# Kernel tuning notes

Hardware: AMD Instinct MI355X
Metric: run time of the kernel (lower is better)

## Reference

```python
import jax, jax.numpy as jnp
import numpy as np

N = 50000      # query points
M = 50000      # support points
KNN = 32       # neighbors per query
K = 15         # kernel points
C_IN = 64
C_OUT = 128
RADIUS = 2.5
KP_EXTENT = 1.2


def setup_inputs() -> dict:
    key = jax.random.key(0)
    ks = jax.random.split(key, 6)
    q_pts = jax.random.uniform(ks[0], (N, 3), dtype=jnp.float32)
    s_pts = jax.random.uniform(ks[1], (M, 3), dtype=jnp.float32)
    s_feats = jax.random.normal(ks[2], (M, C_IN), dtype=jnp.float32)
    # index M refers to the appended shadow point/feature row
    neigh_inds = jax.random.randint(ks[3], (N, KNN), 0, M + 1, dtype=jnp.int32)
    weights = jax.random.normal(ks[4], (K, C_IN, C_OUT), dtype=jnp.float32) * 0.05
    kernel_points = (jax.random.uniform(ks[5], (K, 3), dtype=jnp.float32) * 2.0 - 1.0) * RADIUS
    return {"q_pts": q_pts, "s_pts": s_pts, "s_feats": s_feats,
            "neigh_inds": neigh_inds, "weights": weights,
            "kernel_points": kernel_points}


def reference(q_pts, s_pts, s_feats, neigh_inds, weights, kernel_points):
    # append shadow point far away and zero shadow feature row
    s_pts_pad = jnp.concatenate([s_pts, jnp.full((1, 3), 1e6, s_pts.dtype)], axis=0)
    s_feats_pad = jnp.concatenate(
        [s_feats, jnp.zeros((1, s_feats.shape[1]), s_feats.dtype)], axis=0)

    neigh_pts = s_pts_pad[neigh_inds] - q_pts[:, None, :]       # (n, k, 3)
    neigh_feats = s_feats_pad[neigh_inds]                        # (n, k, c_in)

    diff = neigh_pts[:, :, None, :] - kernel_points[None, None]  # (n, k, K, 3)
    sq_dist = jnp.sum(diff * diff, axis=-1) + 1e-8               # (n, k, K)

    # linear kernel-point influence
    h = jnp.clip(1.0 - jnp.sqrt(sq_dist) / KP_EXTENT, 0.0)       # (n, k, K)

    # aggregate neighbor feats per kernel point, then apply per-kernel weights
    kernel_feats = jnp.einsum('nke,nkc->nec', h, neigh_feats)    # (n, K, c_in)
    q_feats = jnp.einsum('nec,eco->no', kernel_feats, weights)   # (n, c_out)

    # normalize by number of valid (non-shadow, sum>0) neighbors
    neighbor_num = jnp.sum(jnp.sum(neigh_feats, axis=-1) > 0, axis=-1)
    neighbor_num = jnp.maximum(neighbor_num, 1).astype(q_feats.dtype)[:, None]
    return q_feats / neighbor_num
```

## Files before the change

### kernel.cpp

```cpp
#include <hip/hip_runtime.h>


namespace {
constexpr int NQ   = 50000;
constexpr int MS   = 50000;
constexpr int KNN  = 32;
constexpr int KP   = 15;
constexpr int CIN  = 64;
constexpr int COUT = 128;
constexpr int QB   = 32;
constexpr int ROWS = KP * CIN;
constexpr int RND  = 3;
constexpr int RE   = 5;
constexpr int KBR  = (RE * CIN) / 32;
constexpr int KBT  = ROWS / 32;
constexpr int NT   = COUT / 16;
constexpr int ASTR = RE * CIN + 4;
constexpr float KP_EXT_INV = 1.0f / 1.2f;
constexpr size_t WS_HI   = 200704;
constexpr size_t WS_LO   = WS_HI + (size_t)ROWS * COUT * 2;
constexpr size_t WS_NEED = WS_LO + (size_t)ROWS * COUT * 2;
constexpr int OF_H   = 0;
constexpr int OF_DX  = 5280;
constexpr int OF_CPK = 6048;
constexpr int OF_KP  = 6304;
}

typedef __attribute__((ext_vector_type(8))) short short8;
typedef __attribute__((ext_vector_type(4))) float f32x4;
typedef __attribute__((ext_vector_type(4))) unsigned int u32x4;

__device__ __forceinline__ short f32_bf16(float x) {
    unsigned u = __builtin_bit_cast(unsigned, x);
    u = u + 0x7fffu + ((u >> 16) & 1u);
    return (short)(u >> 16);
}
__device__ __forceinline__ float bf16_f32(short h) {
    unsigned u = ((unsigned)(unsigned short)h) << 16;
    return __builtin_bit_cast(float, u);
}
__device__ __forceinline__ unsigned pack_hilo(float x) {
    unsigned xu = __builtin_bit_cast(unsigned, x);
    unsigned r  = xu + 0x7fffu + ((xu >> 16) & 1u);
    unsigned hi = r & 0xffff0000u;
    float lof = x - __builtin_bit_cast(float, hi);
    unsigned lu = __builtin_bit_cast(unsigned, lof);
    unsigned r2 = lu + 0x7fffu + ((lu >> 16) & 1u);
    return hi | (r2 >> 16);
}
__device__ __forceinline__ unsigned permb(unsigned a, unsigned b, unsigned sel) {
#if __has_builtin(__builtin_amdgcn_perm)
    return __builtin_amdgcn_perm(a, b, sel);
#else
    if (sel == 0x07060302u) return (a & 0xffff0000u) | (b >> 16);
    return (a << 16) | (b & 0xffffu);
#endif
}
__device__ __forceinline__ void unpack_a(uint4 a, uint4 b, short8& hi, short8& lo) {
    u32x4 h, l;
    h[0] = permb(a.y, a.x, 0x07060302u); l[0] = permb(a.y, a.x, 0x05040100u);
    h[1] = permb(a.w, a.z, 0x07060302u); l[1] = permb(a.w, a.z, 0x05040100u);
    h[2] = permb(b.y, b.x, 0x07060302u); l[2] = permb(b.y, b.x, 0x05040100u);
    h[3] = permb(b.w, b.z, 0x07060302u); l[3] = permb(b.w, b.z, 0x05040100u);
    hi = __builtin_bit_cast(short8, h);
    lo = __builtin_bit_cast(short8, l);
}

__global__ __launch_bounds__(256)
void prep_kernel(const float* __restrict__ s_feats, const float* __restrict__ W,
                 float* __restrict__ rs, short* __restrict__ whi, short* __restrict__ wlo)
{
    int b = blockIdx.x;
    if (b < 60) {
        int wv = threadIdx.x >> 6, lane = threadIdx.x & 63;
        int id = b * 4 + wv;
        int t = id / KBT, kb = id % KBT;
        short8 hi8, lo8;
        #pragma unroll
        for (int j = 0; j < 8; ++j) {
            int row = kb * 32 + ((lane >> 4) & 3) * 8 + j;
            int col = t * 16 + (lane & 15);
            float x = W[(size_t)row * COUT + col];
            short h = f32_bf16(x);
            hi8[j] = h;
            lo8[j] = f32_bf16(x - bf16_f32(h));
        }
        ((short8*)whi)[id * 64 + lane] = hi8;
        ((short8*)wlo)[id * 64 + lane] = lo8;
    } else {
        int tdx = (b - 60) * 256 + threadIdx.x;
        int row = tdx >> 3, l8 = tdx & 7;
        if (row < MS) {
            const float4* p = (const float4*)(s_feats + (size_t)row * CIN + l8 * 8);
            float4 a = p[0], c = p[1];
            float s = ((a.x + a.y) + (a.z + a.w)) + ((c.x + c.y) + (c.z + c.w));
            s += __shfl_xor(s, 1);
            s += __shfl_xor(s, 2);
            s += __shfl_xor(s, 4);
            if (l8 == 0) rs[row] = s;
        }
    }
}

__global__ __launch_bounds__(512, 4)
void kpconv_mfma(const float* __restrict__ q_pts,
                 const float* __restrict__ s_pts,
                 const float* __restrict__ s_feats,
                 const int*   __restrict__ neigh,
                 const float* __restrict__ kpts,
                 const float* __restrict__ rowsum,
                 const short* __restrict__ whi,
                 const short* __restrict__ wlo,
                 float*       __restrict__ out)
{
    __shared__ __align__(16) unsigned int smem[QB * ASTR];
    __shared__ float norm_s[QB];

    float* smf   = (float*)smem;
    const int tid  = threadIdx.x;
    const int lane = tid & 63;
    const int wv   = tid >> 6;
    const int blk  = blockIdx.x;
    const int k32  = lane & 31;
    const int half = lane >> 5;
    const int quad = lane >> 4;

    float* hbase = smf + OF_H + wv * 660;
    float* dx_b  = smf + OF_DX + wv * 96;
    int*   cpk   = (int*)(smf + OF_CPK) + wv * 32;
    float* kp_s  = smf + OF_KP;

    if (tid < KP * 3) kp_s[tid] = kpts[tid];
    if (lane < 20) hbase[640 + lane] = 0.0f;
    __syncthreads();

    float kfv[4][KP];

    #pragma unroll
    for (int j = 0; j < 4; ++j) {
        const int q  = wv * 4 + j;
        const int n  = blk * QB + q;
        const int nc = n < NQ ? n : NQ - 1;
        const float qx = q_pts[nc * 3 + 0];
        const float qy = q_pts[nc * 3 + 1];
        const float qz = q_pts[nc * 3 + 2];

        int idx = MS;
        bool flag = false;
        if (lane < KNN) {
            idx = neigh[nc * KNN + k32];
            bool valid = idx < MS;
            int  ic    = valid ? idx : MS - 1;
            float px = s_pts[ic * 3 + 0];
            float py = s_pts[ic * 3 + 1];
            float pz = s_pts[ic * 3 + 2];
            dx_b[k32 * 3 + 0] = valid ? px - qx : 1e6f;
            dx_b[k32 * 3 + 1] = valid ? py - qy : 1e6f;
            dx_b[k32 * 3 + 2] = valid ? pz - qz : 1e6f;
            flag = valid && (rowsum[ic] > 0.0f);
        }
        {
            unsigned long long b = __ballot(flag);
            int cnt = (int)__popcll(b);
            if (lane == 0) norm_s[q] = 1.0f / (float)(cnt > 1 ? cnt : 1);
        }
        __builtin_amdgcn_wave_barrier();

        const float dx = dx_b[k32 * 3 + 0];
        const float dy = dx_b[k32 * 3 + 1];
        const float dz = dx_b[k32 * 3 + 2];
        float om = 0.0f;
        #pragma unroll
        for (int p = 0; p < 8; ++p) {
            const int e = (p << 1) + half;
            if (e < KP) {
                float ax = dx - kp_s[e * 3 + 0];
                float ay = dy - kp_s[e * 3 + 1];
                float az = dz - kp_s[e * 3 + 2];
                float d2 = ax * ax + ay * ay + az * az + 1e-8f;
                float hh = 1.0f - sqrtf(d2) * KP_EXT_INV;
                hh = hh > 0.0f ? hh : 0.0f;
                hbase[k32 * 20 + e] = hh;
                om = fmaxf(om, hh);
            }
        }
        om = fmaxf(om, __shfl_xor(om, 32));
        unsigned int kmask = (unsigned int)__ballot(om > 0.0f);
        int nv = __popc(kmask);

        if (lane < KNN) {
            bool bit = (kmask >> k32) & 1u;
            int pos = bit ? __popc(kmask & ((1u << k32) - 1u))
                          : nv + __popc((~kmask) & ((1u << k32) - 1u));
            cpk[pos] = bit ? ((idx << 6) | k32) : 32;
        }
        __builtin_amdgcn_wave_barrier();

        #pragma unroll
        for (int e = 0; e < KP; ++e) kfv[j][e] = 0.0f;
        const int nvr = (nv + 3) & ~3;
        for (int base = 0; base < nvr; base += 4) {
            int pk[4];
            float nf[4];
            #pragma unroll
            for (int u = 0; u < 4; ++u) pk[u] = __builtin_amdgcn_readfirstlane(cpk[base + u]);
            #pragma unroll
            for (int u = 0; u < 4; ++u) nf[u] = s_feats[(size_t)(pk[u] >> 6) * CIN + lane];
            #pragma unroll
            for (int u = 0; u < 4; ++u) {
                const float4* hr = (const float4*)(hbase + (pk[u] & 63) * 20);
                float4 h0 = hr[0], h1 = hr[1], h2 = hr[2], h3 = hr[3];
                float f = nf[u];
                kfv[j][0]  += h0.x * f;  kfv[j][1]  += h0.y * f;
                kfv[j][2]  += h0.z * f;  kfv[j][3]  += h0.w * f;
                kfv[j][4]  += h1.x * f;  kfv[j][5]  += h1.y * f;
                kfv[j][6]  += h1.z * f;  kfv[j][7]  += h1.w * f;
                kfv[j][8]  += h2.x * f;  kfv[j][9]  += h2.y * f;
                kfv[j][10] += h2.z * f;  kfv[j][11] += h2.w * f;
                kfv[j][12] += h3.x * f;  kfv[j][13] += h3.y * f;
                kfv[j][14] += h3.z * f;
            }
        }
    }

    const short8* wh = (const short8*)whi;
    const short8* wl = (const short8*)wlo;
    f32x4 acc0 = {0.f, 0.f, 0.f, 0.f};
    f32x4 acc1 = {0.f, 0.f, 0.f, 0.f};
    const int qA = lane & 15;

    #pragma unroll
    for (int r = 0; r < RND; ++r) {
        __syncthreads();
        #pragma unroll
        for (int j = 0; j < 4; ++j) {
            const int q = wv * 4 + j;
            #pragma unroll
            for (int e5 = 0; e5 < RE; ++e5) {
                smem[q * ASTR + e5 * CIN + lane] = pack_hilo(kfv[j][r * RE + e5]);
            }
        }
        __syncthreads();

        #pragma unroll 2
        for (int kb = 0; kb < KBR; ++kb) {
            const uint4* a0p = (const uint4*)(smem + qA * ASTR + kb * 32 + quad * 8);
            uint4 a0 = a0p[0], a0b = a0p[1];
            const uint4* a1p = (const uint4*)(smem + (16 + qA) * ASTR + kb * 32 + quad * 8);
            uint4 a1 = a1p[0], a1b = a1p[1];
            short8 ah0, al0, ah1, al1;
            unpack_a(a0, a0b, ah0, al0);
            unpack_a(a1, a1b, ah1, al1);

            const int kbg = r * KBR + kb;
            short8 bh = wh[(wv * KBT + kbg) * 64 + lane];
            short8 bl = wl[(wv * KBT + kbg) * 64 + lane];

            acc0 = __builtin_amdgcn_mfma_f32_16x16x32_bf16(ah0, bh, acc0, 0, 0, 0);
            acc1 = __builtin_amdgcn_mfma_f32_16x16x32_bf16(ah1, bh, acc1, 0, 0, 0);
            acc0 = __builtin_amdgcn_mfma_f32_16x16x32_bf16(ah0, bl, acc0, 0, 0, 0);
            acc1 = __builtin_amdgcn_mfma_f32_16x16x32_bf16(ah1, bl, acc1, 0, 0, 0);
            acc0 = __builtin_amdgcn_mfma_f32_16x16x32_bf16(al0, bh, acc0, 0, 0, 0);
            acc1 = __builtin_amdgcn_mfma_f32_16x16x32_bf16(al1, bh, acc1, 0, 0, 0);
        }
    }

    const int oc = lane & 15;
    #pragma unroll
    for (int rr = 0; rr < 4; ++rr) {
        int qm0 = quad * 4 + rr;
        int qm1 = 16 + qm0;
        int n0 = blk * QB + qm0;
        int n1 = blk * QB + qm1;
        if (n0 < NQ) out[(size_t)n0 * COUT + wv * 16 + oc] = acc0[rr] * norm_s[qm0];
        if (n1 < NQ) out[(size_t)n1 * COUT + wv * 16 + oc] = acc1[rr] * norm_s[qm1];
    }
}

__global__ __launch_bounds__(256, 6)
void kpconv_fallback(const float* __restrict__ q_pts,
                     const float* __restrict__ s_pts,
                     const float* __restrict__ s_feats,
                     const int*   __restrict__ neigh,
                     const float* __restrict__ W,
                     const float* __restrict__ kpts,
                     float*       __restrict__ out)
{
    constexpr int QBF = 16, CHUNK_I = 320, NPAIR = 160;
    __shared__ __align__(16) float smem[NPAIR * 32];
    __shared__ float norm_s[QBF];
    float (*h_lds)[KNN][20] = (float (*)[KNN][20])smem;
    float (*dxyz)[KNN][3]   = (float (*)[KNN][3])(smem + 2560);
    int*   idxl             = (int*)(smem + 2944);
    float* kp_s             = smem + 3072;

    const int tid = threadIdx.x, lane = tid & 63, wv = tid >> 6, blk = blockIdx.x;
    const int k32 = lane & 31, half = lane >> 5;
    if (tid < KP * 3) kp_s[tid] = kpts[tid];
    __syncthreads();
    float kfv[4][KP];

    #pragma unroll
    for (int j = 0; j < 4; ++j) {
        const int q = wv * 4 + j, n = blk * QBF + q;
        const float qx = q_pts[n*3], qy = q_pts[n*3+1], qz = q_pts[n*3+2];
        if (lane < KNN) {
            int idx = neigh[n * KNN + k32];
            idxl[wv * KNN + k32] = idx;
            bool valid = idx < MS;
            int ic = valid ? idx : MS - 1;
            dxyz[wv][k32][0] = valid ? s_pts[ic*3]   - qx : 1e6f;
            dxyz[wv][k32][1] = valid ? s_pts[ic*3+1] - qy : 1e6f;
            dxyz[wv][k32][2] = valid ? s_pts[ic*3+2] - qz : 1e6f;
        }
        __builtin_amdgcn_wave_barrier();
        const float dx = dxyz[wv][k32][0], dy = dxyz[wv][k32][1], dz = dxyz[wv][k32][2];
        float om = 0.0f;
        #pragma unroll
        for (int p = 0; p < 8; ++p) {
            const int e = (p << 1) + half;
            if (e < KP) {
                float ax = dx - kp_s[e*3], ay = dy - kp_s[e*3+1], az = dz - kp_s[e*3+2];
                float hh = 1.0f - sqrtf(ax*ax + ay*ay + az*az + 1e-8f) * KP_EXT_INV;
                hh = hh > 0.0f ? hh : 0.0f;
                h_lds[wv][k32][e] = hh;
                om = fmaxf(om, hh);
            }
        }
        om = fmaxf(om, __shfl_xor(om, 32));
        unsigned int kmask = (unsigned int)__ballot(om > 0.0f);
        __builtin_amdgcn_wave_barrier();
        {
            int idx = idxl[wv * KNN + k32];
            bool valid = idx < MS;
            int ic = valid ? idx : MS - 1;
            const float4* rp = (const float4*)(s_feats + (size_t)ic * CIN + half * 32);
            float4 s4 = rp[0];
            #pragma unroll
            for (int t = 1; t < 8; ++t) { float4 a = rp[t]; s4.x+=a.x; s4.y+=a.y; s4.z+=a.z; s4.w+=a.w; }
            float s = (s4.x + s4.y) + (s4.z + s4.w);
            s += __shfl_xor(s, 32);
            unsigned long long b = __ballot(valid && (s > 0.0f));
            int cnt = (int)(__popcll(b) >> 1);
            if (lane == 0) norm_s[q] = 1.0f / (float)(cnt > 1 ? cnt : 1);
        }
        #pragma unroll
        for (int e = 0; e < KP; ++e) kfv[j][e] = 0.0f;
        unsigned int mk = kmask;
        while (mk) {
            int k = __builtin_ctz(mk); mk &= mk - 1;
            int idx2 = idxl[wv * KNN + k];
            int ic2 = idx2 < MS ? idx2 : MS - 1;
            float nf = s_feats[(size_t)ic2 * CIN + lane];
            const float4* hr = (const float4*)(&h_lds[wv][k][0]);
            float4 h0 = hr[0], h1 = hr[1], h2 = hr[2], h3 = hr[3];
            kfv[j][0]+=h0.x*nf; kfv[j][1]+=h0.y*nf; kfv[j][2]+=h0.z*nf; kfv[j][3]+=h0.w*nf;
            kfv[j][4]+=h1.x*nf; kfv[j][5]+=h1.y*nf; kfv[j][6]+=h1.z*nf; kfv[j][7]+=h1.w*nf;
            kfv[j][8]+=h2.x*nf; kfv[j][9]+=h2.y*nf; kfv[j][10]+=h2.z*nf; kfv[j][11]+=h2.w*nf;
            kfv[j][12]+=h3.x*nf; kfv[j][13]+=h3.y*nf; kfv[j][14]+=h3.z*nf;
        }
    }

    const int o4 = tid & 31, qi = tid >> 5, q0 = qi * 2, q1 = q0 + 1;
    float4 tot0 = make_float4(0,0,0,0), tot1 = make_float4(0,0,0,0);
    #pragma unroll
    for (int r = 0; r < 3; ++r) {
        __syncthreads();
        #pragma unroll
        for (int j = 0; j < 4; ++j) {
            const int q = wv * 4 + j;
            #pragma unroll
            for (int e5 = 0; e5 < 5; ++e5) {
                int i = e5 * CIN + lane, pr = i >> 1, m = pr & 14;
                smem[pr * 32 + ((q ^ m) << 1) + (i & 1)] = kfv[j][r * 5 + e5];
            }
        }
        __syncthreads();
        const float* wb = W + (size_t)(r * CHUNK_I) * COUT + (o4 << 2);
        float4 acc0 = make_float4(0,0,0,0), acc1 = make_float4(0,0,0,0);
        #pragma unroll 4
        for (int p = 0; p < NPAIR; ++p) {
            float4 kk = *(const float4*)(smem + p * 32 + ((q0 ^ (p & 14)) << 1));
            float4 w0 = *(const float4*)(wb + (size_t)(2*p) * COUT);
            float4 w1 = *(const float4*)(wb + (size_t)(2*p+1) * COUT);
            acc0.x+=w0.x*kk.x; acc0.y+=w0.y*kk.x; acc0.z+=w0.z*kk.x; acc0.w+=w0.w*kk.x;
            acc1.x+=w0.x*kk.z; acc1.y+=w0.y*kk.z; acc1.z+=w0.z*kk.z; acc1.w+=w0.w*kk.z;
            acc0.x+=w1.x*kk.y; acc0.y+=w1.y*kk.y; acc0.z+=w1.z*kk.y; acc0.w+=w1.w*kk.y;
            acc1.x+=w1.x*kk.w; acc1.y+=w1.y*kk.w; acc1.z+=w1.z*kk.w; acc1.w+=w1.w*kk.w;
        }
        tot0.x+=acc0.x; tot0.y+=acc0.y; tot0.z+=acc0.z; tot0.w+=acc0.w;
        tot1.x+=acc1.x; tot1.y+=acc1.y; tot1.z+=acc1.z; tot1.w+=acc1.w;
    }
    const float nm0 = norm_s[q0], nm1 = norm_s[q1];
    const size_t base = (size_t)(blk * QBF) * COUT + (o4 << 2);
    *(float4*)(out + base + (size_t)q0 * COUT) =
        make_float4(tot0.x*nm0, tot0.y*nm0, tot0.z*nm0, tot0.w*nm0);
    *(float4*)(out + base + (size_t)q1 * COUT) =
        make_float4(tot1.x*nm1, tot1.y*nm1, tot1.z*nm1, tot1.w*nm1);
}

extern "C" void kernel_launch(void* const* d_in, const int* in_sizes, int n_in,
                              void* d_out, int out_size, void* d_ws, size_t ws_size,
                              hipStream_t stream) {
    const float* q_pts   = (const float*)d_in[0];
    const float* s_pts   = (const float*)d_in[1];
    const float* s_feats = (const float*)d_in[2];
    const int*   neigh   = (const int*)d_in[3];
    const float* W       = (const float*)d_in[4];
    const float* kpts    = (const float*)d_in[5];
    float* outp = (float*)d_out;

    if (ws_size >= WS_NEED) {
        float* rs  = (float*)d_ws;
        short* whi = (short*)((char*)d_ws + WS_HI);
        short* wlo = (short*)((char*)d_ws + WS_LO);
        int rs_blocks = (MS * 8 + 255) / 256;
        hipLaunchKernelGGL(prep_kernel, dim3(60 + rs_blocks), dim3(256), 0, stream,
                           s_feats, W, rs, whi, wlo);
        hipLaunchKernelGGL(kpconv_mfma, dim3((NQ + QB - 1) / QB), dim3(512), 0, stream,
                           q_pts, s_pts, s_feats, neigh, kpts, rs, whi, wlo, outp);
    } else {
        hipLaunchKernelGGL(kpconv_fallback, dim3(NQ / 16), dim3(256), 0, stream,
                           q_pts, s_pts, s_feats, neigh, W, kpts, outp);
    }
}
```

Measured before the change: 163.8 us.

## Compute per-query kernel-point aggregation with bf16x3 MFMA instead of scalar FMAs

Replaces the scalar loop that accumulates influence times neighbor features with a 16x16x32 MFMA per query, using hi/lo bf16 splitting for near-fp32 accuracy. Influence weights are written transposed into shared memory, and neighbor feature rows are gathered per lane. A new prep kernel pre-packs all support features into hi/lo bf16 pairs in the workspace when it is large enough. This drops the neighbor-compaction skip of zero-influence neighbors and adds extra gather traffic and pack work in exchange for matrix-core throughput.

Result: slower. 207.5 us (+26.7%).

```diff
diff --git a/kernel.cpp b/kernel.cpp
--- a/kernel.cpp
+++ b/kernel.cpp
@@ -14,16 +14,19 @@
 constexpr int RE   = 5;
 constexpr int KBR  = (RE * CIN) / 32;
 constexpr int KBT  = ROWS / 32;
-constexpr int NT   = COUT / 16;
 constexpr int ASTR = RE * CIN + 4;
 constexpr float KP_EXT_INV = 1.0f / 1.2f;
-constexpr size_t WS_HI   = 200704;
-constexpr size_t WS_LO   = WS_HI + (size_t)ROWS * COUT * 2;
-constexpr size_t WS_NEED = WS_LO + (size_t)ROWS * COUT * 2;
-constexpr int OF_H   = 0;
-constexpr int OF_DX  = 5280;
-constexpr int OF_CPK = 6048;
-constexpr int OF_KP  = 6304;
+constexpr int OF_HT  = 0;
+constexpr int OF_DX  = 4608;
+constexpr int OF_IDX = 5376;
+constexpr int OF_KP  = 5632;
+constexpr size_t WSF_FPK = 200704;
+constexpr size_t WSF_HI  = WSF_FPK + (size_t)MS * CIN * 4;
+constexpr size_t WSF_LO  = WSF_HI + (size_t)ROWS * COUT * 2;
+constexpr size_t WSF_END = WSF_LO + (size_t)ROWS * COUT * 2;
+constexpr size_t WSB_HI  = 200704;
+constexpr size_t WSB_LO  = 446464;
+constexpr size_t WSB_END = 692224;
 }
 
 typedef __attribute__((ext_vector_type(8))) short short8;
@@ -56,7 +59,7 @@
     return (a << 16) | (b & 0xffffu);
 #endif
 }
-__device__ __forceinline__ void unpack_a(uint4 a, uint4 b, short8& hi, short8& lo) {
+__device__ __forceinline__ void unpack8(uint4 a, uint4 b, short8& hi, short8& lo) {
     u32x4 h, l;
     h[0] = permb(a.y, a.x, 0x07060302u); l[0] = permb(a.y, a.x, 0x05040100u);
     h[1] = permb(a.w, a.z, 0x07060302u); l[1] = permb(a.w, a.z, 0x05040100u);
@@ -67,8 +70,41 @@
 }
 
 __global__ __launch_bounds__(256)
-void prep_kernel(const float* __restrict__ s_feats, const float* __restrict__ W,
-                 float* __restrict__ rs, short* __restrict__ whi, short* __restrict__ wlo)
+void prep_full(const float* __restrict__ s_feats, const float* __restrict__ W,
+               float* __restrict__ rs, unsigned* __restrict__ fpk,
+               short* __restrict__ whi, short* __restrict__ wlo)
+{
+    int b = blockIdx.x;
+    if (b < 60) {
+        int wv = threadIdx.x >> 6, lane = threadIdx.x & 63;
+        int id = b * 4 + wv;
+        int t = id / KBT, kb = id % KBT;
+        short8 hi8, lo8;
+        #pragma unroll
+        for (int j = 0; j < 8; ++j) {
+            int row = kb * 32 + ((lane >> 4) & 3) * 8 + j;
+            int col = t * 16 + (lane & 15);
+            float x = W[(size_t)row * COUT + col];
+            short h = f32_bf16(x);
+            hi8[j] = h;
+            lo8[j] = f32_bf16(x - bf16_f32(h));
+        }
+        ((short8*)whi)[id * 64 + lane] = hi8;
+        ((short8*)wlo)[id * 64 + lane] = lo8;
+    } else {
+        int t = (b - 60) * 256 + threadIdx.x;
+        float x = s_feats[t];
+        fpk[t] = pack_hilo(x);
+        float s = x;
+        s += __shfl_xor(s, 1);  s += __shfl_xor(s, 2);  s += __shfl_xor(s, 4);
+        s += __shfl_xor(s, 8);  s += __shfl_xor(s, 16); s += __shfl_xor(s, 32);
+        if ((t & 63) == 0) rs[t >> 6] = s;
+    }
+}
+
+__global__ __launch_bounds__(256)
+void prep_basic(const float* __restrict__ s_feats, const float* __restrict__ W,
+                float* __restrict__ rs, short* __restrict__ whi, short* __restrict__ wlo)
 {
     int b = blockIdx.x;
     if (b < 60) {
@@ -102,6 +138,7 @@
     }
 }
 
+template<bool PREPACKED>
 __global__ __launch_bounds__(512, 4)
 void kpconv_mfma(const float* __restrict__ q_pts,
                  const float* __restrict__ s_pts,
@@ -109,6 +146,7 @@
                  const int*   __restrict__ neigh,
                  const float* __restrict__ kpts,
                  const float* __restrict__ rowsum,
+                 const unsigned* __restrict__ fpk,
                  const short* __restrict__ whi,
                  const short* __restrict__ wlo,
                  float*       __restrict__ out)
@@ -116,7 +154,7 @@
     __shared__ __align__(16) unsigned int smem[QB * ASTR];
     __shared__ float norm_s[QB];
 
-    float* smf   = (float*)smem;
+    float* smf = (float*)smem;
     const int tid  = threadIdx.x;
     const int lane = tid & 63;
     const int wv   = tid >> 6;
@@ -124,17 +162,17 @@
     const int k32  = lane & 31;
     const int half = lane >> 5;
     const int quad = lane >> 4;
-
-    float* hbase = smf + OF_H + wv * 660;
-    float* dx_b  = smf + OF_DX + wv * 96;
-    int*   cpk   = (int*)(smf + OF_CPK) + wv * 32;
-    float* kp_s  = smf + OF_KP;
+    const int c15  = lane & 15;
+
+    unsigned* hT  = smem + OF_HT + wv * 576;
+    float*    dxb = smf + OF_DX + wv * 96;
+    int*      idxl = (int*)(smf + OF_IDX) + wv * 32;
+    float*    kp_s = smf + OF_KP;
 
     if (tid < KP * 3) kp_s[tid] = kpts[tid];
-    if (lane < 20) hbase[640 + lane] = 0.0f;
     __syncthreads();
 
-    float kfv[4][KP];
+    unsigned pkf[4][4][4];
 
     #pragma unroll
     for (int j = 0; j < 4; ++j) {
@@ -145,18 +183,18 @@
         const float qy = q_pts[nc * 3 + 1];
         const float qz = q_pts[nc * 3 + 2];
 
-        int idx = MS;
         bool flag = false;
         if (lane < KNN) {
-            idx = neigh[nc * KNN + k32];
+            int idx = neigh[nc * KNN + k32];
             bool valid = idx < MS;
             int  ic    = valid ? idx : MS - 1;
+            idxl[k32] = ic;
             float px = s_pts[ic * 3 + 0];
             float py = s_pts[ic * 3 + 1];
             float pz = s_pts[ic * 3 + 2];
-            dx_b[k32 * 3 + 0] = valid ? px - qx : 1e6f;
-            dx_b[k32 * 3 + 1] = valid ? py - qy : 1e6f;
-            dx_b[k32 * 3 + 2] = valid ? pz - qz : 1e6f;
+            dxb[k32 * 3 + 0] = valid ? px - qx : 1e6f;
+            dxb[k32 * 3 + 1] = valid ? py - qy : 1e6f;
+            dxb[k32 * 3 + 2] = valid ? pz - qz : 1e6f;
             flag = valid && (rowsum[ic] > 0.0f);
         }
         {
@@ -166,10 +204,9 @@
         }
         __builtin_amdgcn_wave_barrier();
 
-        const float dx = dx_b[k32 * 3 + 0];
-        const float dy = dx_b[k32 * 3 + 1];
-        const float dz = dx_b[k32 * 3 + 2];
-        float om = 0.0f;
+        const float dx = dxb[k32 * 3 + 0];
+        const float dy = dxb[k32 * 3 + 1];
+        const float dz = dxb[k32 * 3 + 2];
         #pragma unroll
         for (int p = 0; p < 8; ++p) {
             const int e = (p << 1) + half;
@@ -180,46 +217,48 @@
                 float d2 = ax * ax + ay * ay + az * az + 1e-8f;
                 float hh = 1.0f - sqrtf(d2) * KP_EXT_INV;
                 hh = hh > 0.0f ? hh : 0.0f;
-                hbase[k32 * 20 + e] = hh;
-                om = fmaxf(om, hh);
+                hT[e * 36 + k32] = pack_hilo(hh);
             }
         }
-        om = fmaxf(om, __shfl_xor(om, 32));
-        unsigned int kmask = (unsigned int)__ballot(om > 0.0f);
-        int nv = __popc(kmask);
-
-        if (lane < KNN) {
-            bool bit = (kmask >> k32) & 1u;
-            int pos = bit ? __popc(kmask & ((1u << k32) - 1u))
-                          : nv + __popc((~kmask) & ((1u << k32) - 1u));
-            cpk[pos] = bit ? ((idx << 6) | k32) : 32;
-        }
         __builtin_amdgcn_wave_barrier();
 
-        #pragma unroll
-        for (int e = 0; e < KP; ++e) kfv[j][e] = 0.0f;
-        const int nvr = (nv + 3) & ~3;
-        for (int base = 0; base < nvr; base += 4) {
-            int pk[4];
-            float nf[4];
+        const uint4* ap = (const uint4*)(hT + c15 * 36 + quad * 8);
+        uint4 A0 = ap[0], A1 = ap[1];
+        short8 ahi, alo;
+        unpack8(A0, A1, ahi, alo);
+
+        const int r0 = idxl[quad * 8 + 0], r1 = idxl[quad * 8 + 1];
+        const int r2 = idxl[quad * 8 + 2], r3 = idxl[quad * 8 + 3];
+        const int r4 = idxl[quad * 8 + 4], r5 = idxl[quad * 8 + 5];
+        const int r6 = idxl[quad * 8 + 6], r7 = idxl[quad * 8 + 7];
+
+        #pragma unroll
+        for (int t = 0; t < 4; ++t) {
+            const int co = t * 16 + c15;
+            unsigned d0, d1, d2_, d3, d4, d5, d6, d7;
+            if (PREPACKED) {
+                d0 = fpk[(size_t)r0 * CIN + co]; d1 = fpk[(size_t)r1 * CIN + co];
+                d2_= fpk[(size_t)r2 * CIN + co]; d3 = fpk[(size_t)r3 * CIN + co];
+                d4 = fpk[(size_t)r4 * CIN + co]; d5 = fpk[(size_t)r5 * CIN + co];
+                d6 = fpk[(size_t)r6 * CIN + co]; d7 = fpk[(size_t)r7 * CIN + co];
+            } else {
+                d0 = pack_hilo(s_feats[(size_t)r0 * CIN + co]);
+                d1 = pack_hilo(s_feats[(size_t)r1 * CIN + co]);
+                d2_= pack_hilo(s_feats[(size_t)r2 * CIN + co]);
+                d3 = pack_hilo(s_feats[(size_t)r3 * CIN + co]);
+                d4 = pack_hilo(s_feats[(size_t)r4 * CIN + co]);
+                d5 = pack_hilo(s_feats[(size_t)r5 * CIN + co]);
+                d6 = pack_hilo(s_feats[(size_t)r6 * CIN + co]);
+                d7 = pack_hilo(s_feats[(size_t)r7 * CIN + co]);
+            }
+            short8 bhi, blo;
+            unpack8(make_uint4(d0, d1, d2_, d3), make_uint4(d4, d5, d6, d7), bhi, blo);
+            f32x4 a = {0.f, 0.f, 0.f, 0.f};
+            a = __builtin_amdgcn_mfma_f32_16x16x32_bf16(ahi, bhi, a, 0, 0, 0);
+            a = __builtin_amdgcn_mfma_f32_16x16x32_bf16(ahi, blo, a, 0, 0, 0);
+            a = __builtin_amdgcn_mfma_f32_16x16x32_bf16(alo, bhi, a, 0, 0, 0);
             #pragma unroll
-            for (int u = 0; u < 4; ++u) pk[u] = __builtin_amdgcn_readfirstlane(cpk[base + u]);
-            #pragma unroll
-            for (int u = 0; u < 4; ++u) nf[u] = s_feats[(size_t)(pk[u] >> 6) * CIN + lane];
-            #pragma unroll
-            for (int u = 0; u < 4; ++u) {
-                const float4* hr = (const float4*)(hbase + (pk[u] & 63) * 20);
-                float4 h0 = hr[0], h1 = hr[1], h2 = hr[2], h3 = hr[3];
-                float f = nf[u];
-                kfv[j][0]  += h0.x * f;  kfv[j][1]  += h0.y * f;
-                kfv[j][2]  += h0.z * f;  kfv[j][3]  += h0.w * f;
-                kfv[j][4]  += h1.x * f;  kfv[j][5]  += h1.y * f;
-                kfv[j][6]  += h1.z * f;  kfv[j][7]  += h1.w * f;
-                kfv[j][8]  += h2.x * f;  kfv[j][9]  += h2.y * f;
-                kfv[j][10] += h2.z * f;  kfv[j][11] += h2.w * f;
-                kfv[j][12] += h3.x * f;  kfv[j][13] += h3.y * f;
-                kfv[j][14] += h3.z * f;
-            }
+            for (int rr = 0; rr < 4; ++rr) pkf[j][t][rr] = pack_hilo(a[rr]);
         }
     }
 
@@ -227,17 +266,23 @@
     const short8* wl = (const short8*)wlo;
     f32x4 acc0 = {0.f, 0.f, 0.f, 0.f};
     f32x4 acc1 = {0.f, 0.f, 0.f, 0.f};
-    const int qA = lane & 15;
+    const int qA = c15;
 
     #pragma unroll
     for (int r = 0; r < RND; ++r) {
         __syncthreads();
         #pragma unroll
         for (int j = 0; j < 4; ++j) {
-            const int q = wv * 4 + j;
+            const int qrow = (4 * wv + j) * ASTR;
             #pragma unroll
-            for (int e5 = 0; e5 < RE; ++e5) {
-                smem[q * ASTR + e5 * CIN + lane] = pack_hilo(kfv[j][r * RE + e5]);
+            for (int t = 0; t < 4; ++t) {
+                #pragma unroll
+                for (int rr = 0; rr < 4; ++rr) {
+                    const int e = quad * 4 + rr;
+                    if (e >= r * RE && e < r * RE + RE) {
+                        smem[qrow + (e - r * RE) * CIN + t * 16 + c15] = pkf[j][t][rr];
+                    }
+                }
             }
         }
         __syncthreads();
@@ -249,8 +294,8 @@
             const uint4* a1p = (const uint4*)(smem + (16 + qA) * ASTR + kb * 32 + quad * 8);
             uint4 a1 = a1p[0], a1b = a1p[1];
             short8 ah0, al0, ah1, al1;
-            unpack_a(a0, a0b, ah0, al0);
-            unpack_a(a1, a1b, ah1, al1);
+            unpack8(a0, a0b, ah0, al0);
+            unpack8(a1, a1b, ah1, al1);
 
             const int kbg = r * KBR + kb;
             short8 bh = wh[(wv * KBT + kbg) * 64 + lane];
@@ -265,7 +310,7 @@
         }
     }
 
-    const int oc = lane & 15;
+    const int oc = c15;
     #pragma unroll
     for (int rr = 0; rr < 4; ++rr) {
         int qm0 = quad * 4 + rr;
@@ -410,15 +455,29 @@
     const float* kpts    = (const float*)d_in[5];
     float* outp = (float*)d_out;
 
-    if (ws_size >= WS_NEED) {
+    dim3 mgrid((NQ + QB - 1) / QB);
+    dim3 mblock(512);
+
+    if (ws_size >= WSF_END) {
+        float*    rs  = (float*)d_ws;
+        unsigned* fpk = (unsigned*)((char*)d_ws + WSF_FPK);
+        short*    whi = (short*)((char*)d_ws + WSF_HI);
+        short*    wlo = (short*)((char*)d_ws + WSF_LO);
+        int grid = 60 + (MS * CIN) / 256;
+        hipLaunchKernelGGL(prep_full, dim3(grid), dim3(256), 0, stream,
+                           s_feats, W, rs, fpk, whi, wlo);
+        hipLaunchKernelGGL(kpconv_mfma<true>, mgrid, mblock, 0, stream,
+                           q_pts, s_pts, s_feats, neigh, kpts, rs, fpk, whi, wlo, outp);
+    } else if (ws_size >= WSB_END) {
         float* rs  = (float*)d_ws;
-        short* whi = (short*)((char*)d_ws + WS_HI);
-        short* wlo = (short*)((char*)d_ws + WS_LO);
+        short* whi = (short*)((char*)d_ws + WSB_HI);
+        short* wlo = (short*)((char*)d_ws + WSB_LO);
         int rs_blocks = (MS * 8 + 255) / 256;
-        hipLaunchKernelGGL(prep_kernel, dim3(60 + rs_blocks), dim3(256), 0, stream,
+        hipLaunchKernelGGL(prep_basic, dim3(60 + rs_blocks), dim3(256), 0, stream,
                            s_feats, W, rs, whi, wlo);
-        hipLaunchKernelGGL(kpconv_mfma, dim3((NQ + QB - 1) / QB), dim3(512), 0, stream,
-                           q_pts, s_pts, s_feats, neigh, kpts, rs, whi, wlo, outp);
+        hipLaunchKernelGGL(kpconv_mfma<false>, mgrid, mblock, 0, stream,
+                           q_pts, s_pts, s_feats, neigh, kpts, rs,
+                           (const unsigned*)nullptr, whi, wlo, outp);
     } else {
         hipLaunchKernelGGL(kpconv_fallback, dim3(NQ / 16), dim3(256), 0, stream,
                            q_pts, s_pts, s_feats, neigh, W, kpts, outp);
```
